# Performance work log

Hardware: AMD Instinct MI355X
Metric: run time of the kernel (lower is better)

## Reference

```python
import jax, jax.numpy as jnp
import numpy as np

B, D, Q, E, H, V = 32, 1024, 64, 384, 384, 50000
PAD = 0
EPS = 1e-12


def setup_inputs() -> dict:
    key = jax.random.key(0)
    ks = jax.random.split(key, 13)
    documents = jax.random.randint(ks[0], (B, D), 1, V)
    doc_lens = jax.random.randint(ks[1], (B,), D // 2, D + 1)
    doc_valid = jnp.arange(D)[None, :] < doc_lens[:, None]
    documents = jnp.where(doc_valid, documents, PAD)
    doc_masks = doc_valid.astype(jnp.float32)[:, :, None]
    querys = jax.random.randint(ks[2], (B, Q), 1, V)
    query_lens = jax.random.randint(ks[3], (B,), Q // 2, Q + 1)
    q_valid = jnp.arange(Q)[None, :] < query_lens[:, None]
    querys = jnp.where(q_valid, querys, PAD)
    query_masks = q_valid.astype(jnp.float32)[:, :, None]
    answers = documents[:, :1]  # guaranteed present in each doc
    emb = jax.random.uniform(ks[4], (V + 1, E), jnp.float32, -0.05, 0.05)
    emb = emb.at[PAD].set(0.0)
    gw = lambda k, s: jax.random.normal(k, s, jnp.float32) * 0.05
    w_ih_f = gw(ks[5], (3 * H, E)); w_hh_f = gw(ks[6], (3 * H, H))
    b_ih_f = gw(ks[7], (3 * H,)); b_hh_f = gw(ks[8], (3 * H,))
    w_ih_b = gw(ks[9], (3 * H, E)); w_hh_b = gw(ks[10], (3 * H, H))
    b_ih_b = gw(ks[11], (3 * H,)); b_hh_b = gw(ks[12], (3 * H,))
    return dict(documents=documents, doc_lens=doc_lens, doc_masks=doc_masks,
                querys=querys, query_lens=query_lens, query_masks=query_masks,
                answers=answers, emb=emb,
                w_ih_f=w_ih_f, w_hh_f=w_hh_f, b_ih_f=b_ih_f, b_hh_f=b_hh_f,
                w_ih_b=w_ih_b, w_hh_b=w_hh_b, b_ih_b=b_ih_b, b_hh_b=b_hh_b)


def _gru_dir(x, w_ih, w_hh, b_ih, b_hh):
    # x: [B,T,E] -> outputs [B,T,H]; torch GRU cell math
    Bn = x.shape[0]
    Hn = w_hh.shape[1]
    xp = jnp.einsum('bte,ge->btg', x, w_ih) + b_ih  # precompute input projections [B,T,3H]

    def step(h, g):
        gh = h @ w_hh.T + b_hh
        i_r, i_z, i_n = jnp.split(g, 3, axis=-1)
        h_r, h_z, h_n = jnp.split(gh, 3, axis=-1)
        r = jax.nn.sigmoid(i_r + h_r)
        z = jax.nn.sigmoid(i_z + h_z)
        n = jnp.tanh(i_n + r * h_n)
        hn = (1.0 - z) * n + z * h
        return hn, hn

    h0 = jnp.zeros((Bn, Hn), x.dtype)
    _, out = jax.lax.scan(step, h0, jnp.swapaxes(xp, 0, 1))
    return jnp.swapaxes(out, 0, 1)


def _rev_within_len(x, lens):
    # reverse each sequence only over its valid prefix (emulates packed bwd GRU)
    T = x.shape[1]
    t = jnp.arange(T)
    idx = jnp.where(t[None, :] < lens[:, None], lens[:, None] - 1 - t[None, :], t[None, :])
    return jnp.take_along_axis(x, idx[:, :, None], axis=1)


def _bigru(x, lens, valid, pf, pb):
    out_f = _gru_dir(x, *pf)
    out_b = _rev_within_len(_gru_dir(_rev_within_len(x, lens), *pb), lens)
    out = jnp.concatenate([out_f, out_b], axis=-1)
    return out * valid[:, :, None]  # unpack pads with zeros


def _softmax_mask(x, mask, axis):
    shift = jnp.max(x, axis=axis, keepdims=True)
    e = jnp.exp(x - shift) * mask
    return e / (jnp.sum(e, axis=axis, keepdims=True) + EPS)


def reference(documents, doc_lens, doc_masks, querys, query_lens, query_masks, answers,
              emb, w_ih_f, w_hh_f, b_ih_f, b_hh_f, w_ih_b, w_hh_b, b_ih_b, b_hh_b):
    doc_valid = doc_masks[..., 0]
    q_valid = query_masks[..., 0]
    doc_h = _bigru(emb[documents], doc_lens, doc_valid,
                   (w_ih_f, w_hh_f, b_ih_f, b_hh_f), (w_ih_b, w_hh_b, b_ih_b, b_hh_b))
    q_h = _bigru(emb[querys], query_lens, q_valid,
                 (w_ih_f, w_hh_f, b_ih_f, b_hh_f), (w_ih_b, w_hh_b, b_ih_b, b_hh_b))
    scores = jnp.einsum('bdh,bqh->bdq', doc_h, q_h)          # IndiATT_output
    pair_mask = jnp.einsum('bdo,bqo->bdq', doc_masks, query_masks)
    alpha = _softmax_mask(scores, pair_mask, axis=1)
    beta = _softmax_mask(scores, pair_mask, axis=2)
    beta_aver = jnp.sum(beta, axis=1) / doc_lens[:, None].astype(scores.dtype)  # [B,Q]
    s = jnp.einsum('bdq,bq->bd', alpha, beta_aver)            # AoA_output squeezed
    probs = jnp.sum(s * (documents == answers).astype(s.dtype), axis=1)

    def pick(doc, sv, vv):
        sc = jnp.zeros(V + 1, s.dtype).at[doc].add(sv * vv)   # segment-sum by word id
        cnt = jnp.zeros(V + 1, s.dtype).at[doc].add(vv)
        return jnp.argmax(jnp.where(cnt > 0, sc, -jnp.inf))

    pred_answers = jax.vmap(pick)(documents, s, doc_valid)
    return probs, pred_answers
```

## Files before the change

### kernel.cpp

```cpp
#include <hip/hip_runtime.h>
#include <hip/hip_bf16.h>
#include <stdint.h>

#define EPSV 1e-12f
#define NB 32
#define DD 1024
#define QQ 64
#define EE 384
#define HH 384
#define NW 12

typedef __attribute__((ext_vector_type(4))) float f32x4;
typedef __attribute__((ext_vector_type(8))) __bf16 bf16x8;
typedef __attribute__((ext_vector_type(4))) unsigned short u16x4;
typedef unsigned short u16;

static __device__ __forceinline__ u16 f2bf(float f) {
  union { float f; uint32_t u; } v; v.f = f;
  uint32_t u = v.u;
  return (u16)((u + 0x7fffu + ((u >> 16) & 1u)) >> 16);
}

static __device__ __forceinline__ f32x4 MFMA(bf16x8 a, bf16x8 b, f32x4 c) {
  return __builtin_amdgcn_mfma_f32_16x16x32_bf16(a, b, c, 0, 0, 0);
}

__global__ __launch_bounds__(256) void k_emb(const int* __restrict__ doc, const int* __restrict__ qry,
                                             const float* __restrict__ emb, u16* __restrict__ embx) {
  int i = blockIdx.x * 256 + threadIdx.x;
  int row = i / 96, e4 = i - row * 96;
  int tok = (row < NB * DD) ? doc[row] : qry[row - NB * DD];
  float4 v = ((const float4*)(emb + (size_t)tok * EE))[e4];
  u16x4 o; o.x = f2bf(v.x); o.y = f2bf(v.y); o.z = f2bf(v.z); o.w = f2bf(v.w);
  *(u16x4*)(embx + (size_t)row * EE + e4 * 4) = o;
}

static __device__ __forceinline__ void grpbar(unsigned* c) {
  __syncthreads();
  if (threadIdx.x == 0) {
    __hip_atomic_fetch_add(c, 1u, __ATOMIC_RELEASE, __HIP_MEMORY_SCOPE_AGENT);
    while (__hip_atomic_load(c, __ATOMIC_RELAXED, __HIP_MEMORY_SCOPE_AGENT) < (unsigned)NW)
      __builtin_amdgcn_s_sleep(2);
    (void)__hip_atomic_load(c, __ATOMIC_ACQUIRE, __HIP_MEMORY_SCOPE_AGENT);
  }
  __syncthreads();
}

__global__ __launch_bounds__(256) void k_rec(
    const u16* __restrict__ embx,
    const int* __restrict__ doc_lens, const int* __restrict__ q_lens,
    const float* __restrict__ w_ih_f, const float* __restrict__ w_hh_f,
    const float* __restrict__ b_ih_f, const float* __restrict__ b_hh_f,
    const float* __restrict__ w_ih_b, const float* __restrict__ w_hh_b,
    const float* __restrict__ b_ih_b, const float* __restrict__ b_hh_b,
    u16* __restrict__ doc_h, u16* __restrict__ q_h,
    u16* __restrict__ h_bc, unsigned* __restrict__ cnts) {
  __shared__ u16 wfrag[73728];
  __shared__ float h_own[32][33];
  __shared__ int lensh[32];

  const int grp = blockIdx.x / NW;
  const int wg = blockIdx.x - grp * NW;
  const int corpus = grp >> 1, dir = grp & 1;
  const int T = corpus ? QQ : DD;
  const int* lens = corpus ? q_lens : doc_lens;
  const float* w_ih = dir ? w_ih_b : w_ih_f;
  const float* w_hh = dir ? w_hh_b : w_hh_f;
  const float* b_ih = dir ? b_ih_b : b_ih_f;
  const float* b_hh = dir ? b_hh_b : b_hh_f;
  u16* out = corpus ? q_h : doc_h;
  const u16* ex_base = embx + (corpus ? (size_t)NB * DD * EE : 0);
  u16* hb = h_bc + (size_t)grp * (2 * NB * HH);
  unsigned* cnt = cnts + grp * 1056;
  const int tid = threadIdx.x;

  if (tid < 32) lensh[tid] = lens[tid];
  for (int idx = tid; idx < 73728; idx += 256) {
    int nt = idx / 12288;
    int rem = idx - nt * 12288;
    int ks = rem >> 9;
    int le = rem & 511;
    int lane_ = le >> 3, i = le & 7;
    int g = nt >> 1, js_ = nt & 1;
    int colw = lane_ & 15, khiw = lane_ >> 4;
    int k = ks * 32 + khiw * 8 + i;
    int rowg = g * 384 + wg * 32 + js_ * 16 + colw;
    float v = (k < 384) ? w_ih[rowg * 384 + k] : w_hh[rowg * 384 + (k - 384)];
    wfrag[idx] = f2bf(v);
  }
  for (int idx = tid; idx < 32 * 33; idx += 256) (&h_own[0][0])[idx] = 0.f;
  for (int idx = tid; idx < 1024; idx += 256) {
    int b = idx >> 5, jl_ = idx & 31;
    hb[b * HH + wg * 32 + jl_] = 0;
  }
  grpbar(cnt + 0);

  const int lane = tid & 63, wv = tid >> 6;
  const int mt = wv >> 1, js = wv & 1;
  const int col = lane & 15, khi = lane >> 4;
  const int jg = wg * 32 + js * 16 + col;
  const float bias_r = b_ih[jg] + b_hh[jg];
  const float bias_z = b_ih[384 + jg] + b_hh[384 + jg];
  const float bias_in = b_ih[768 + jg];
  const float bias_hn = b_hh[768 + jg];
  const int b_x = mt * 16 + col;
  const int len_x = lensh[b_x];
  const int bh0 = mt * 16 + khi * 4;
  int len_h[4];
#pragma unroll
  for (int r = 0; r < 4; ++r) len_h[r] = lensh[bh0 + r];
  const u16* exrow = ex_base + (size_t)b_x * T * EE + khi * 8;
  u16* outp = out + (size_t)dir * HH + jg;
  const int jl = js * 16 + col;

  auto trow_of = [&](int s) -> int { return dir ? ((s < len_x) ? (len_x - 1 - s) : s) : s; };
  auto load_ax = [&](bf16x8* ax, int s) {
    const u16* axp = exrow + (size_t)trow_of(s) * EE;
#pragma unroll
    for (int ks = 0; ks < 12; ++ks) ax[ks] = *(const bf16x8*)(axp + ks * 32);
  };

  bf16x8 axA[12], axB[12];
  load_ax(axA, 0);

  auto step = [&](int s, bf16x8* axc, bf16x8* axn) {
    const int p = s & 1;
    const u16* rbuf = hb + p * (NB * HH);
    u16* wbuf = hb + (p ^ 1) * (NB * HH);
    const u16* ahp = rbuf + b_x * HH + khi * 8;
    bf16x8 ah[12];
#pragma unroll
    for (int ks = 0; ks < 12; ++ks) ah[ks] = *(const bf16x8*)(ahp + ks * 32);
    f32x4 acc_r{0.f, 0.f, 0.f, 0.f};
    f32x4 acc_z = acc_r, acc_nx = acc_r, acc_nh = acc_r;
#pragma unroll
    for (int ks = 0; ks < 12; ++ks) {
      bf16x8 br = *(const bf16x8*)&wfrag[((js) * 24 + ks) * 512 + lane * 8];
      bf16x8 bz = *(const bf16x8*)&wfrag[((2 + js) * 24 + ks) * 512 + lane * 8];
      bf16x8 bn = *(const bf16x8*)&wfrag[((4 + js) * 24 + ks) * 512 + lane * 8];
      acc_r = MFMA(axc[ks], br, acc_r);
      acc_z = MFMA(axc[ks], bz, acc_z);
      acc_nx = MFMA(axc[ks], bn, acc_nx);
    }
#pragma unroll
    for (int ks = 0; ks < 12; ++ks) {
      bf16x8 br = *(const bf16x8*)&wfrag[((js) * 24 + 12 + ks) * 512 + lane * 8];
      bf16x8 bz = *(const bf16x8*)&wfrag[((2 + js) * 24 + 12 + ks) * 512 + lane * 8];
      bf16x8 bn = *(const bf16x8*)&wfrag[((4 + js) * 24 + 12 + ks) * 512 + lane * 8];
      acc_r = MFMA(ah[ks], br, acc_r);
      acc_z = MFMA(ah[ks], bz, acc_z);
      acc_nh = MFMA(ah[ks], bn, acc_nh);
    }
#pragma unroll
    for (int r = 0; r < 4; ++r) {
      const int b = bh0 + r;
      float rg = 1.f / (1.f + __expf(-(acc_r[r] + bias_r)));
      float zg = 1.f / (1.f + __expf(-(acc_z[r] + bias_z)));
      float ng = tanhf(acc_nx[r] + bias_in + rg * (acc_nh[r] + bias_hn));
      float hp = h_own[b][jl];
      float hn = (1.f - zg) * ng + zg * hp;
      h_own[b][jl] = hn;
      u16 hq = f2bf(hn);
      wbuf[b * HH + jg] = hq;
      const int len = len_h[r];
      const int tro = dir ? ((s < len) ? (len - 1 - s) : s) : s;
      outp[((size_t)b * T + tro) * (2 * HH)] = hq;
    }
    if (s + 1 < T) load_ax(axn, s + 1);
    grpbar(cnt + 1 + s);
  };

  for (int s = 0; s < T; s += 2) {
    step(s, axA, axB);
    step(s + 1, axB, axA);
  }
}

__global__ __launch_bounds__(256) void k_scores(
    const u16* __restrict__ doc_h, const u16* __restrict__ q_h,
    const int* __restrict__ doc_lens, const int* __restrict__ q_lens,
    float* __restrict__ SM, float* __restrict__ rowmax, float* __restrict__ rowsum) {
  const int b = blockIdx.x >> 4, dblk = blockIdx.x & 15;
  const int tid = threadIdx.x, lane = tid & 63, wv = tid >> 6;
  const int col = lane & 15, khi = lane >> 4;
  const int dlen = doc_lens[b], qlen = q_lens[b];
  const u16* dp = doc_h + ((size_t)(b * DD + dblk * 64 + wv * 16 + col)) * (2 * HH) + khi * 8;
  const u16* qp = q_h + (size_t)b * QQ * (2 * HH);
  f32x4 acc[4];
#pragma unroll
  for (int nt = 0; nt < 4; ++nt) acc[nt] = f32x4{0.f, 0.f, 0.f, 0.f};
  for (int ks = 0; ks < 24; ++ks) {
    bf16x8 av = *(const bf16x8*)(dp + ks * 32);
#pragma unroll
    for (int nt = 0; nt < 4; ++nt) {
      bf16x8 bv = *(const bf16x8*)(qp + (size_t)(nt * 16 + col) * (2 * HH) + ks * 32 + khi * 8);
      acc[nt] = MFMA(av, bv, acc[nt]);
    }
  }
  const int d0 = dblk * 64 + wv * 16 + khi * 4;
  float* smb = SM + (size_t)b * DD * QQ;
#pragma unroll
  for (int r = 0; r < 4; ++r) {
    const int d = d0 + r;
    const bool dv = d < dlen;
    float v[4];
#pragma unroll
    for (int nt = 0; nt < 4; ++nt) {
      const int q = nt * 16 + col;
      v[nt] = (dv && q < qlen) ? acc[nt][r] : 0.f;
      smb[(size_t)d * QQ + q] = v[nt];
    }
    float mx = fmaxf(fmaxf(v[0], v[1]), fmaxf(v[2], v[3]));
#pragma unroll
    for (int off = 1; off < 16; off <<= 1) mx = fmaxf(mx, __shfl_xor(mx, off, 64));
    float sm = 0.f;
#pragma unroll
    for (int nt = 0; nt < 4; ++nt) {
      const int q = nt * 16 + col;
      if (dv && q < qlen) sm += __expf(v[nt] - mx);
    }
#pragma unroll
    for (int off = 1; off < 16; off <<= 1) sm += __shfl_xor(sm, off, 64);
    if (col == 0) { rowmax[b * DD + d] = mx; rowsum[b * DD + d] = sm; }
  }
}

__global__ __launch_bounds__(256) void k_cols(
    const float* __restrict__ SM, const float* __restrict__ rowmax, const float* __restrict__ rowsum,
    const int* __restrict__ doc_lens, const int* __restrict__ q_lens,
    float* __restrict__ colmax, float* __restrict__ colsum, float* __restrict__ bav) {
  const int b = blockIdx.x, tid = threadIdx.x;
  const int q = tid & 63, dg = tid >> 6;
  __shared__ float red[4][64];
  __shared__ float cmx[64];
  const float* smb = SM + (size_t)b * DD * QQ;
  float cm = -3.0e38f;
  for (int d = dg; d < DD; d += 4) cm = fmaxf(cm, smb[(size_t)d * QQ + q]);
  red[dg][q] = cm;
  __syncthreads();
  if (tid < 64) cmx[tid] = fmaxf(fmaxf(red[0][tid], red[1][tid]), fmaxf(red[2][tid], red[3][tid]));
  __syncthreads();
  const int dlen = doc_lens[b];
  const bool qv = q < q_lens[b];
  const float cmq = cmx[q];
  float cs = 0.f, ba = 0.f;
  for (int d = dg; d < DD; d += 4) {
    if (qv && d < dlen) {
      float v = smb[(size_t)d * QQ + q];
      cs += __expf(v - cmq);
      ba += __expf(v - rowmax[b * DD + d]) / (rowsum[b * DD + d] + EPSV);
    }
  }
  __syncthreads();
  red[dg][q] = cs;
  __syncthreads();
  float cst = 0.f;
  if (tid < 64) cst = red[0][tid] + red[1][tid] + red[2][tid] + red[3][tid];
  __syncthreads();
  red[dg][q] = ba;
  __syncthreads();
  if (tid < 64) {
    float bat = red[0][tid] + red[1][tid] + red[2][tid] + red[3][tid];
    colmax[b * QQ + tid] = cmx[tid];
    colsum[b * QQ + tid] = cst;
    bav[b * QQ + tid] = bat / (float)dlen;
  }
}

__global__ __launch_bounds__(256) void k_s(
    const float* __restrict__ SM, const float* __restrict__ colmax, const float* __restrict__ colsum,
    const float* __restrict__ bav, const int* __restrict__ doc_lens, const int* __restrict__ q_lens,
    const int* __restrict__ documents, const int* __restrict__ answers,
    float* __restrict__ sc, float* __restrict__ cnt_tok, float* __restrict__ dout) {
  const int b = blockIdx.x >> 2, dblk = blockIdx.x & 3;
  const int tid = threadIdx.x;
  __shared__ float cm[64], cs[64], bv[64];
  __shared__ int qm[64];
  if (tid < 64) {
    cm[tid] = colmax[b * QQ + tid];
    cs[tid] = colsum[b * QQ + tid];
    bv[tid] = bav[b * QQ + tid];
    qm[tid] = (tid < q_lens[b]) ? 1 : 0;
  }
  __syncthreads();
  const int d = dblk * 256 + tid;
  const bool dv = d < doc_lens[b];
  const float* smr = SM + ((size_t)b * DD + d) * QQ;
  float sd = 0.f;
#pragma unroll
  for (int q = 0; q < 64; ++q) {
    float e = (dv && qm[q]) ? __expf(smr[q] - cm[q]) : 0.f;
    sd += e / (cs[q] + EPSV) * bv[q];
  }
  const int tok = documents[b * DD + d];
  if (tok == answers[b]) atomicAdd(&dout[b], sd);
  if (dv) {
    atomicAdd(&sc[(size_t)b * 50001 + tok], sd);
    atomicAdd(&cnt_tok[(size_t)b * 50001 + tok], 1.0f);
  }
}

__global__ __launch_bounds__(256) void k_pred(
    const float* __restrict__ sc, const float* __restrict__ cnt_tok, float* __restrict__ dout) {
  const int b = blockIdx.x, tid = threadIdx.x;
  __shared__ float bvs[256];
  __shared__ int bis[256];
  float bvv = -3.0e38f;
  int bii = 0x7fffffff;
  for (int i = tid; i < 50001; i += 256) {
    if (cnt_tok[(size_t)b * 50001 + i] > 0.f) {
      float v = sc[(size_t)b * 50001 + i];
      if (v > bvv) { bvv = v; bii = i; }
    }
  }
  bvs[tid] = bvv;
  bis[tid] = bii;
  __syncthreads();
  for (int st = 128; st > 0; st >>= 1) {
    if (tid < st) {
      float v2 = bvs[tid + st];
      int i2 = bis[tid + st];
      if (v2 > bvs[tid] || (v2 == bvs[tid] && i2 < bis[tid])) { bvs[tid] = v2; bis[tid] = i2; }
    }
    __syncthreads();
  }
  if (tid == 0) dout[32 + b] = (float)bis[0];
}

extern "C" void kernel_launch(void* const* d_in, const int* in_sizes, int n_in,
                              void* d_out, int out_size, void* d_ws, size_t ws_size,
                              hipStream_t stream) {
  const int* documents = (const int*)d_in[0];
  const int* doc_lens = (const int*)d_in[1];
  const int* querys = (const int*)d_in[3];
  const int* query_lens = (const int*)d_in[4];
  const int* answers = (const int*)d_in[6];
  const float* emb = (const float*)d_in[7];
  const float* w_ih_f = (const float*)d_in[8];
  const float* w_hh_f = (const float*)d_in[9];
  const float* b_ih_f = (const float*)d_in[10];
  const float* b_hh_f = (const float*)d_in[11];
  const float* w_ih_b = (const float*)d_in[12];
  const float* w_hh_b = (const float*)d_in[13];
  const float* b_ih_b = (const float*)d_in[14];
  const float* b_hh_b = (const float*)d_in[15];
  float* dout = (float*)d_out;
  char* ws = (char*)d_ws;

  size_t o = 0;
  auto alloc = [&](size_t bytes) { size_t r = o; o += (bytes + 255) & ~(size_t)255; return r; };
  size_t o_embx = alloc((size_t)34816 * 384 * 2);
  size_t o_doch = alloc((size_t)NB * DD * 768 * 2);
  size_t o_qh   = alloc((size_t)NB * QQ * 768 * 2);
  size_t o_hbc  = alloc((size_t)4 * 2 * NB * HH * 2);
  size_t o_cnt  = alloc((size_t)4 * 1056 * 4);
  size_t o_SM   = alloc((size_t)NB * DD * QQ * 4);
  size_t o_rmax = alloc((size_t)NB * DD * 4);
  size_t o_rsum = alloc((size_t)NB * DD * 4);
  size_t o_cmax = alloc((size_t)NB * QQ * 4);
  size_t o_csum = alloc((size_t)NB * QQ * 4);
  size_t o_bav  = alloc((size_t)NB * QQ * 4);
  size_t o_sc   = alloc((size_t)NB * 50001 * 4);
  size_t o_ctk  = alloc((size_t)NB * 50001 * 4);
  (void)ws_size; (void)in_sizes; (void)n_in; (void)out_size;

  hipMemsetAsync(ws + o_cnt, 0, (size_t)4 * 1056 * 4, stream);
  hipMemsetAsync(ws + o_sc, 0, (o_ctk - o_sc) + (size_t)NB * 50001 * 4, stream);
  hipMemsetAsync(d_out, 0, 64 * sizeof(float), stream);

  k_emb<<<13056, 256, 0, stream>>>(documents, querys, emb, (u16*)(ws + o_embx));
  k_rec<<<48, 256, 0, stream>>>((u16*)(ws + o_embx), doc_lens, query_lens,
                                w_ih_f, w_hh_f, b_ih_f, b_hh_f,
                                w_ih_b, w_hh_b, b_ih_b, b_hh_b,
                                (u16*)(ws + o_doch), (u16*)(ws + o_qh),
                                (u16*)(ws + o_hbc), (unsigned*)(ws + o_cnt));
  k_scores<<<512, 256, 0, stream>>>((u16*)(ws + o_doch), (u16*)(ws + o_qh), doc_lens, query_lens,
                                    (float*)(ws + o_SM), (float*)(ws + o_rmax), (float*)(ws + o_rsum));
  k_cols<<<32, 256, 0, stream>>>((float*)(ws + o_SM), (float*)(ws + o_rmax), (float*)(ws + o_rsum),
                                 doc_lens, query_lens,
                                 (float*)(ws + o_cmax), (float*)(ws + o_csum), (float*)(ws + o_bav));
  k_s<<<128, 256, 0, stream>>>((float*)(ws + o_SM), (float*)(ws + o_cmax), (float*)(ws + o_csum),
                               (float*)(ws + o_bav), doc_lens, query_lens, documents, answers,
                               (float*)(ws + o_sc), (float*)(ws + o_ctk), dout);
  k_pred<<<32, 256, 0, stream>>>((float*)(ws + o_sc), (float*)(ws + o_ctk), dout);
}
```

Before: 6.411 ms.

## Replace release/acquire group barrier with sc1 stores/loads and padded counters

The cross-workgroup barrier in the GRU recurrence now uses relaxed atomics, with hidden-state exchange done through sc1 (cache-coherent) global stores and loads instead of release/acquire fences. Counters are padded to 64 bytes so each step's counter sits on its own cache line. The previous hidden state is kept in registers instead of shared memory, and the next step's input prefetch is issued before the hidden-state loads. This targets the per-step fence and cache-flush cost on the serial 1024-step critical path. It relies on sc1 semantics and explicit waitcnt for correctness across workgroups, which is fragile.

```diff
diff --git a/kernel.cpp b/kernel.cpp
--- a/kernel.cpp
+++ b/kernel.cpp
@@ -13,6 +13,7 @@
 typedef __attribute__((ext_vector_type(4))) float f32x4;
 typedef __attribute__((ext_vector_type(8))) __bf16 bf16x8;
 typedef __attribute__((ext_vector_type(4))) unsigned short u16x4;
+typedef __attribute__((ext_vector_type(4))) int i32x4;
 typedef unsigned short u16;
 
 static __device__ __forceinline__ u16 f2bf(float f) {
@@ -23,6 +24,13 @@
 
 static __device__ __forceinline__ f32x4 MFMA(bf16x8 a, bf16x8 b, f32x4 c) {
   return __builtin_amdgcn_mfma_f32_16x16x32_bf16(a, b, c, 0, 0, 0);
+}
+
+static __device__ __forceinline__ void st_short_sc(u16* p, u16 v) {
+  asm volatile("global_store_short %0, %1, off sc1" :: "v"(p), "v"((uint32_t)v) : "memory");
+}
+static __device__ __forceinline__ void ld_b128_sc(const u16* p, i32x4& d) {
+  asm volatile("global_load_dwordx4 %0, %1, off sc1" : "=v"(d) : "v"(p) : "memory");
 }
 
 __global__ __launch_bounds__(256) void k_emb(const int* __restrict__ doc, const int* __restrict__ qry,
@@ -33,17 +41,6 @@
   float4 v = ((const float4*)(emb + (size_t)tok * EE))[e4];
   u16x4 o; o.x = f2bf(v.x); o.y = f2bf(v.y); o.z = f2bf(v.z); o.w = f2bf(v.w);
   *(u16x4*)(embx + (size_t)row * EE + e4 * 4) = o;
-}
-
-static __device__ __forceinline__ void grpbar(unsigned* c) {
-  __syncthreads();
-  if (threadIdx.x == 0) {
-    __hip_atomic_fetch_add(c, 1u, __ATOMIC_RELEASE, __HIP_MEMORY_SCOPE_AGENT);
-    while (__hip_atomic_load(c, __ATOMIC_RELAXED, __HIP_MEMORY_SCOPE_AGENT) < (unsigned)NW)
-      __builtin_amdgcn_s_sleep(2);
-    (void)__hip_atomic_load(c, __ATOMIC_ACQUIRE, __HIP_MEMORY_SCOPE_AGENT);
-  }
-  __syncthreads();
 }
 
 __global__ __launch_bounds__(256) void k_rec(
@@ -56,7 +53,6 @@
     u16* __restrict__ doc_h, u16* __restrict__ q_h,
     u16* __restrict__ h_bc, unsigned* __restrict__ cnts) {
   __shared__ u16 wfrag[73728];
-  __shared__ float h_own[32][33];
   __shared__ int lensh[32];
 
   const int grp = blockIdx.x / NW;
@@ -71,7 +67,7 @@
   u16* out = corpus ? q_h : doc_h;
   const u16* ex_base = embx + (corpus ? (size_t)NB * DD * EE : 0);
   u16* hb = h_bc + (size_t)grp * (2 * NB * HH);
-  unsigned* cnt = cnts + grp * 1056;
+  unsigned* cnt = cnts + (size_t)grp * (1056 * 16);
   const int tid = threadIdx.x;
 
   if (tid < 32) lensh[tid] = lens[tid];
@@ -88,12 +84,18 @@
     float v = (k < 384) ? w_ih[rowg * 384 + k] : w_hh[rowg * 384 + (k - 384)];
     wfrag[idx] = f2bf(v);
   }
-  for (int idx = tid; idx < 32 * 33; idx += 256) (&h_own[0][0])[idx] = 0.f;
   for (int idx = tid; idx < 1024; idx += 256) {
     int b = idx >> 5, jl_ = idx & 31;
-    hb[b * HH + wg * 32 + jl_] = 0;
-  }
-  grpbar(cnt + 0);
+    st_short_sc(hb + b * HH + wg * 32 + jl_, (u16)0);
+  }
+  asm volatile("s_waitcnt vmcnt(0)" ::: "memory");
+  __syncthreads();
+  if (tid == 0) {
+    __hip_atomic_fetch_add(cnt, 1u, __ATOMIC_RELAXED, __HIP_MEMORY_SCOPE_AGENT);
+    while (__hip_atomic_load(cnt, __ATOMIC_RELAXED, __HIP_MEMORY_SCOPE_AGENT) < (unsigned)NW)
+      __builtin_amdgcn_s_sleep(1);
+  }
+  __syncthreads();
 
   const int lane = tid & 63, wv = tid >> 6;
   const int mt = wv >> 1, js = wv & 1;
@@ -111,7 +113,7 @@
   for (int r = 0; r < 4; ++r) len_h[r] = lensh[bh0 + r];
   const u16* exrow = ex_base + (size_t)b_x * T * EE + khi * 8;
   u16* outp = out + (size_t)dir * HH + jg;
-  const int jl = js * 16 + col;
+  f32x4 hprev{0.f, 0.f, 0.f, 0.f};
 
   auto trow_of = [&](int s) -> int { return dir ? ((s < len_x) ? (len_x - 1 - s) : s) : s; };
   auto load_ax = [&](bf16x8* ax, int s) {
@@ -127,10 +129,11 @@
     const int p = s & 1;
     const u16* rbuf = hb + p * (NB * HH);
     u16* wbuf = hb + (p ^ 1) * (NB * HH);
+    if (s + 1 < T) load_ax(axn, s + 1);
+    i32x4 areg[12];
     const u16* ahp = rbuf + b_x * HH + khi * 8;
-    bf16x8 ah[12];
-#pragma unroll
-    for (int ks = 0; ks < 12; ++ks) ah[ks] = *(const bf16x8*)(ahp + ks * 32);
+#pragma unroll
+    for (int ks = 0; ks < 12; ++ks) ld_b128_sc(ahp + ks * 32, areg[ks]);
     f32x4 acc_r{0.f, 0.f, 0.f, 0.f};
     f32x4 acc_z = acc_r, acc_nx = acc_r, acc_nh = acc_r;
 #pragma unroll
@@ -142,14 +145,17 @@
       acc_z = MFMA(axc[ks], bz, acc_z);
       acc_nx = MFMA(axc[ks], bn, acc_nx);
     }
+    asm volatile("s_waitcnt vmcnt(0)" ::: "memory");
+    __builtin_amdgcn_sched_barrier(0);
 #pragma unroll
     for (int ks = 0; ks < 12; ++ks) {
+      bf16x8 af = __builtin_bit_cast(bf16x8, areg[ks]);
       bf16x8 br = *(const bf16x8*)&wfrag[((js) * 24 + 12 + ks) * 512 + lane * 8];
       bf16x8 bz = *(const bf16x8*)&wfrag[((2 + js) * 24 + 12 + ks) * 512 + lane * 8];
       bf16x8 bn = *(const bf16x8*)&wfrag[((4 + js) * 24 + 12 + ks) * 512 + lane * 8];
-      acc_r = MFMA(ah[ks], br, acc_r);
-      acc_z = MFMA(ah[ks], bz, acc_z);
-      acc_nh = MFMA(ah[ks], bn, acc_nh);
+      acc_r = MFMA(af, br, acc_r);
+      acc_z = MFMA(af, bz, acc_z);
+      acc_nh = MFMA(af, bn, acc_nh);
     }
 #pragma unroll
     for (int r = 0; r < 4; ++r) {
@@ -157,17 +163,23 @@
       float rg = 1.f / (1.f + __expf(-(acc_r[r] + bias_r)));
       float zg = 1.f / (1.f + __expf(-(acc_z[r] + bias_z)));
       float ng = tanhf(acc_nx[r] + bias_in + rg * (acc_nh[r] + bias_hn));
-      float hp = h_own[b][jl];
-      float hn = (1.f - zg) * ng + zg * hp;
-      h_own[b][jl] = hn;
+      float hn = (1.f - zg) * ng + zg * hprev[r];
+      hprev[r] = hn;
       u16 hq = f2bf(hn);
-      wbuf[b * HH + jg] = hq;
+      st_short_sc(wbuf + b * HH + jg, hq);
       const int len = len_h[r];
       const int tro = dir ? ((s < len) ? (len - 1 - s) : s) : s;
       outp[((size_t)b * T + tro) * (2 * HH)] = hq;
     }
-    if (s + 1 < T) load_ax(axn, s + 1);
-    grpbar(cnt + 1 + s);
+    asm volatile("s_waitcnt vmcnt(0)" ::: "memory");
+    __syncthreads();
+    if (tid == 0) {
+      unsigned* c = cnt + (size_t)(s + 1) * 16;
+      __hip_atomic_fetch_add(c, 1u, __ATOMIC_RELAXED, __HIP_MEMORY_SCOPE_AGENT);
+      while (__hip_atomic_load(c, __ATOMIC_RELAXED, __HIP_MEMORY_SCOPE_AGENT) < (unsigned)NW)
+        __builtin_amdgcn_s_sleep(1);
+    }
+    __syncthreads();
   };
 
   for (int s = 0; s < T; s += 2) {
@@ -353,7 +365,7 @@
   size_t o_doch = alloc((size_t)NB * DD * 768 * 2);
   size_t o_qh   = alloc((size_t)NB * QQ * 768 * 2);
   size_t o_hbc  = alloc((size_t)4 * 2 * NB * HH * 2);
-  size_t o_cnt  = alloc((size_t)4 * 1056 * 4);
+  size_t o_cnt  = alloc((size_t)4 * 1056 * 16 * 4);
   size_t o_SM   = alloc((size_t)NB * DD * QQ * 4);
   size_t o_rmax = alloc((size_t)NB * DD * 4);
   size_t o_rsum = alloc((size_t)NB * DD * 4);
@@ -364,7 +376,7 @@
   size_t o_ctk  = alloc((size_t)NB * 50001 * 4);
   (void)ws_size; (void)in_sizes; (void)n_in; (void)out_size;
 
-  hipMemsetAsync(ws + o_cnt, 0, (size_t)4 * 1056 * 4, stream);
+  hipMemsetAsync(ws + o_cnt, 0, (size_t)4 * 1056 * 16 * 4, stream);
   hipMemsetAsync(ws + o_sc, 0, (o_ctk - o_sc) + (size_t)NB * 50001 * 4, stream);
   hipMemsetAsync(d_out, 0, 64 * sizeof(float), stream);
 
```

Result: faster. 6.000 ms (-6.4%).
